# Kernel tuning notes

Hardware: AMD Instinct MI355X
Metric: run time of the kernel (lower is better)

Reference implementation:

```python
import jax, jax.numpy as jnp
import numpy as np

DX = 0.1
DY = 0.1
W_B = 1000.0
W_PARALLEL = 1000.0
W_DIV = 100.0
EPS = 1e-10


def setup_inputs() -> dict:
    key = jax.random.key(0)
    k1, k2 = jax.random.split(key)
    outputs = jax.random.normal(k1, (2, 3, 256, 256, 64), dtype=jnp.float32)
    targets = jax.random.normal(k2, (2, 4, 256, 256, 64), dtype=jnp.float32)
    return {"outputs": outputs, "targets": targets}


def _corners(f):
    # 8 shifted views f[..., i:, j:, k:] (with 0 -> [0:-1], 1 -> [1:]) on dims 2,3,4
    s0, s1 = slice(0, -1), slice(1, None)
    return {(i, j, k): f[:, :, (s1 if i else s0), (s1 if j else s0), (s1 if k else s0)]
            for i in (0, 1) for j in (0, 1) for k in (0, 1)}


def _forward(outputs, targets):
    bx_p, by_p, bz_p = outputs[:, 0:1], outputs[:, 1:2], outputs[:, 2:3]
    bx_t, by_t, bz_t = targets[:, 0:1], targets[:, 1:2], targets[:, 2:3]

    loss_b = (jnp.mean((bx_p**2 + by_p**2 - bx_t**2 - by_t**2) ** 2 / (bx_t**2 + by_t**2 + EPS))
              + jnp.mean((bz_p - bz_t) ** 4 / (bz_t**2 + EPS)))
    loss_parallel = jnp.mean((bx_p * by_t - by_p * bx_t) ** 2
                             / (bx_t**2 + by_t**2 + bz_t**2 + EPS))

    bx = _corners(bx_p)
    by = _corners(by_p)
    bz = _corners(bz_p)
    z = _corners(targets[:, 3:4])

    num = (0.25 * (bx[1, 0, 0] + bx[1, 1, 0] + bx[1, 0, 1] + bx[1, 1, 1]) * DY * 0.5 * (z[1, 0, 1] - z[1, 0, 0] + z[1, 1, 1] - z[1, 1, 0])
           - 0.25 * (bx[0, 0, 0] + bx[0, 1, 0] + bx[0, 0, 1] + bx[0, 1, 1]) * DY * 0.5 * (z[0, 0, 1] - z[0, 0, 0] + z[0, 1, 1] - z[0, 1, 0])
           + 0.25 * (by[0, 1, 0] + by[1, 1, 0] + by[0, 1, 1] + by[1, 1, 1]) * DX * 0.5 * (z[0, 1, 1] - z[0, 1, 0] + z[1, 1, 1] - z[1, 1, 0])
           - 0.25 * (by[0, 0, 0] + by[1, 0, 0] + by[0, 0, 1] + by[1, 0, 1]) * DX * 0.5 * (z[0, 0, 1] - z[0, 0, 0] + z[1, 0, 1] - z[1, 0, 0])
           + 0.25 * (bz[0, 0, 1] + bz[0, 1, 1] + bz[1, 0, 1] + bz[1, 1, 1]) * DX * DY
           - 0.25 * (bz[0, 0, 0] + bz[0, 1, 0] + bz[1, 0, 0] + bz[1, 1, 0]) * DX * DY
           + (bx[0, 0, 1] + bx[1, 0, 1] + bx[1, 1, 1]) * DY * (z[0, 0, 1] - z[1, 0, 1]) / 6
           + (bx[0, 1, 1] + bx[1, 1, 1] + bx[1, 0, 1]) * DY * (z[0, 1, 1] - z[1, 1, 1]) / 6
           + (by[1, 0, 1] + by[1, 1, 1] + by[0, 1, 1]) * DX * (z[1, 0, 1] - z[1, 1, 1]) / 6
           + (by[0, 0, 1] + by[0, 1, 1] + by[1, 1, 1]) * DX * (z[0, 0, 1] - z[0, 1, 1]) / 6
           - (bx[0, 0, 0] + bx[1, 0, 0] + bx[1, 1, 0]) * DY * (z[0, 0, 0] - z[1, 0, 0]) / 6
           - (bx[0, 1, 0] + bx[1, 1, 0] + bx[1, 0, 0]) * DY * (z[0, 1, 0] - z[1, 1, 0]) / 6
           - (by[1, 0, 0] + by[1, 1, 0] + by[0, 1, 0]) * DX * (z[1, 0, 0] - z[1, 1, 0]) / 6
           - (by[0, 0, 0] + by[0, 1, 0] + by[1, 1, 0]) * DX * (z[0, 0, 0] - z[0, 1, 0]) / 6)

    bx_c = sum(bx[c] for c in sorted(bx)) * 0.125
    by_c = sum(by[c] for c in sorted(by)) * 0.125
    bz_c = sum(bz[c] for c in sorted(bz)) * 0.125
    den = bx_c**2 + by_c**2 + bz_c**2 + EPS

    loss_div = jnp.mean(num**2 / den) / DX**2 / DY**2

    return (W_B * loss_b + W_PARALLEL * loss_parallel, W_DIV * loss_div)


def reference(outputs, targets):
    return _forward(outputs, targets)
```

## Files before the change

### kernel.cpp

```cpp
#include <hip/hip_runtime.h>

constexpr int B = 2, X = 256, Y = 256, Z = 64;
constexpr int CO = X * Y * Z;
constexpr int YZ = Y * Z;
constexpr long long N_PTS   = (long long)B * X * Y * Z;
constexpr long long M_CELLS = (long long)B * (X-1) * (Y-1) * (Z-1);

constexpr int ROWS = 4;
constexpr int SEGS = Y / ROWS;
constexpr int TPB  = 256;
constexpr int WPB  = TPB / 64;
constexpr int NSEG   = B * SEGS * X;
constexpr int BLOCKS = NSEG / WPB;

#define DXc 0.1f
#define DYc 0.1f
#define EPSc 1e-10f

#define F4C(v, c) (((c) == 0) ? (v).x : ((c) == 1) ? (v).y : ((c) == 2) ? (v).z : (v).w)

__global__ __launch_bounds__(TPB) void loss_main(const float* __restrict__ outs,
                                                 const float* __restrict__ tgts,
                                                 double* __restrict__ partial) {
    const int lane = threadIdx.x & 63;
    const int wv   = threadIdx.x >> 6;
    const int seg  = blockIdx.x * WPB + wv;

    const int b  = seg >> 14;
    const int r  = seg & 16383;
    const int sy = r >> 8;
    const int x  = r & 255;
    const int y0 = sy * ROWS;

    const int row = lane >> 4;
    const int zi  = (lane & 15) << 2;
    const int y_own = y0 + row;
    const int y_up  = (y_own + 1 < Y) ? (y_own + 1) : (Y - 1);

    const float* ob = outs + (size_t)b * 3 * CO;
    const float* tb = tgts + (size_t)b * 4 * CO;
    const int off00 = x * YZ + y_own * Z + zi;
    const int off01 = x * YZ + y_up  * Z + zi;
    const int off10 = off00 + YZ;
    const int off11 = off01 + YZ;

    #define LD4(p, off) (*(const float4*)((p) + (off)))

    double s_pt = 0.0;
    double s_dv = 0.0;

    const float4 obx = LD4(ob, 0 * CO + off00);
    const float4 oby = LD4(ob, 1 * CO + off00);
    const float4 obz = LD4(ob, 2 * CO + off00);
    const float4 tbx = LD4(tb, 0 * CO + off00);
    const float4 tby = LD4(tb, 1 * CO + off00);
    const float4 tbz = LD4(tb, 2 * CO + off00);
    const float4 tzc = LD4(tb, 3 * CO + off00);

    #pragma unroll
    for (int c = 0; c < 4; ++c) {
        const float bxp = F4C(obx, c), byp = F4C(oby, c), bzp = F4C(obz, c);
        const float bxt = F4C(tbx, c), byt = F4C(tby, c), bzt = F4C(tbz, c);
        const float bxt2 = bxt * bxt, byt2 = byt * byt, bzt2 = bzt * bzt;
        const float t1 = bxp * bxp + byp * byp - bxt2 - byt2;
        const float e1 = t1 * t1 / (bxt2 + byt2 + EPSc);
        const float dd = bzp - bzt;
        const float dd2 = dd * dd;
        const float e2 = dd2 * dd2 / (bzt2 + EPSc);
        const float cr = bxp * byt - byp * bxt;
        const float e3 = cr * cr / (bxt2 + byt2 + bzt2 + EPSc);
        s_pt += (double)(e1 + e2 + e3);
    }

    if (x < X - 1) {
        const float4 obx1  = LD4(ob, 0 * CO + off10);
        const float4 oby1  = LD4(ob, 1 * CO + off10);
        const float4 obz1  = LD4(ob, 2 * CO + off10);
        const float4 tzc1  = LD4(tb, 3 * CO + off10);
        const float4 obxy  = LD4(ob, 0 * CO + off01);
        const float4 obyy  = LD4(ob, 1 * CO + off01);
        const float4 obzy  = LD4(ob, 2 * CO + off01);
        const float4 tzcy  = LD4(tb, 3 * CO + off01);
        const float4 obxy1 = LD4(ob, 0 * CO + off11);
        const float4 obyy1 = LD4(ob, 1 * CO + off11);
        const float4 obzy1 = LD4(ob, 2 * CO + off11);
        const float4 tzcy1 = LD4(tb, 3 * CO + off11);

        const float n_obx   = __shfl_down(obx.x,   1);
        const float n_oby   = __shfl_down(oby.x,   1);
        const float n_obz   = __shfl_down(obz.x,   1);
        const float n_tzc   = __shfl_down(tzc.x,   1);
        const float n_obx1  = __shfl_down(obx1.x,  1);
        const float n_oby1  = __shfl_down(oby1.x,  1);
        const float n_obz1  = __shfl_down(obz1.x,  1);
        const float n_tzc1  = __shfl_down(tzc1.x,  1);
        const float n_obxy  = __shfl_down(obxy.x,  1);
        const float n_obyy  = __shfl_down(obyy.x,  1);
        const float n_obzy  = __shfl_down(obzy.x,  1);
        const float n_tzcy  = __shfl_down(tzcy.x,  1);
        const float n_obxy1 = __shfl_down(obxy1.x, 1);
        const float n_obyy1 = __shfl_down(obyy1.x, 1);
        const float n_obzy1 = __shfl_down(obzy1.x, 1);
        const float n_tzcy1 = __shfl_down(tzcy1.x, 1);

        const bool yvalid = (y_own < Y - 1);
        const float SIXTH = 1.0f / 6.0f;

        #pragma unroll
        for (int c = 0; c < 4; ++c) {
            const float bx000 = F4C(obx, c),   bx100 = F4C(obx1, c);
            const float bx010 = F4C(obxy, c),  bx110 = F4C(obxy1, c);
            const float by000 = F4C(oby, c),   by100 = F4C(oby1, c);
            const float by010 = F4C(obyy, c),  by110 = F4C(obyy1, c);
            const float bz000 = F4C(obz, c),   bz100 = F4C(obz1, c);
            const float bz010 = F4C(obzy, c),  bz110 = F4C(obzy1, c);
            const float zc000 = F4C(tzc, c),   zc100 = F4C(tzc1, c);
            const float zc010 = F4C(tzcy, c),  zc110 = F4C(tzcy1, c);

            const float bx001 = (c < 3) ? F4C(obx, c + 1)   : n_obx;
            const float bx101 = (c < 3) ? F4C(obx1, c + 1)  : n_obx1;
            const float bx011 = (c < 3) ? F4C(obxy, c + 1)  : n_obxy;
            const float bx111 = (c < 3) ? F4C(obxy1, c + 1) : n_obxy1;
            const float by001 = (c < 3) ? F4C(oby, c + 1)   : n_oby;
            const float by101 = (c < 3) ? F4C(oby1, c + 1)  : n_oby1;
            const float by011 = (c < 3) ? F4C(obyy, c + 1)  : n_obyy;
            const float by111 = (c < 3) ? F4C(obyy1, c + 1) : n_obyy1;
            const float bz001 = (c < 3) ? F4C(obz, c + 1)   : n_obz;
            const float bz101 = (c < 3) ? F4C(obz1, c + 1)  : n_obz1;
            const float bz011 = (c < 3) ? F4C(obzy, c + 1)  : n_obzy;
            const float bz111 = (c < 3) ? F4C(obzy1, c + 1) : n_obzy1;
            const float zc001 = (c < 3) ? F4C(tzc, c + 1)   : n_tzc;
            const float zc101 = (c < 3) ? F4C(tzc1, c + 1)  : n_tzc1;
            const float zc011 = (c < 3) ? F4C(tzcy, c + 1)  : n_tzcy;
            const float zc111 = (c < 3) ? F4C(tzcy1, c + 1) : n_tzcy1;

            const float num =
                  0.25f * (bx100 + bx110 + bx101 + bx111) * DYc * 0.5f * (zc101 - zc100 + zc111 - zc110)
                - 0.25f * (bx000 + bx010 + bx001 + bx011) * DYc * 0.5f * (zc001 - zc000 + zc011 - zc010)
                + 0.25f * (by010 + by110 + by011 + by111) * DXc * 0.5f * (zc011 - zc010 + zc111 - zc110)
                - 0.25f * (by000 + by100 + by001 + by101) * DXc * 0.5f * (zc001 - zc000 + zc101 - zc100)
                + 0.25f * (bz001 + bz011 + bz101 + bz111) * DXc * DYc
                - 0.25f * (bz000 + bz010 + bz100 + bz110) * DXc * DYc
                + (bx001 + bx101 + bx111) * DYc * (zc001 - zc101) * SIXTH
                + (bx011 + bx111 + bx101) * DYc * (zc011 - zc111) * SIXTH
                + (by101 + by111 + by011) * DXc * (zc101 - zc111) * SIXTH
                + (by001 + by011 + by111) * DXc * (zc001 - zc011) * SIXTH
                - (bx000 + bx100 + bx110) * DYc * (zc000 - zc100) * SIXTH
                - (bx010 + bx110 + bx100) * DYc * (zc010 - zc110) * SIXTH
                - (by100 + by110 + by010) * DXc * (zc100 - zc110) * SIXTH
                - (by000 + by010 + by110) * DXc * (zc000 - zc010) * SIXTH;

            const float bxc = 0.125f * (bx000 + bx100 + bx010 + bx110 + bx001 + bx101 + bx011 + bx111);
            const float byc = 0.125f * (by000 + by100 + by010 + by110 + by001 + by101 + by011 + by111);
            const float bzc = 0.125f * (bz000 + bz100 + bz010 + bz110 + bz001 + bz101 + bz011 + bz111);
            const float den = bxc * bxc + byc * byc + bzc * bzc + EPSc;

            const bool zvalid = (zi + c) < (Z - 1);
            if (yvalid && zvalid) {
                s_dv += (double)(num * num / den);
            }
        }
    }

    for (int off = 32; off > 0; off >>= 1) {
        s_pt += __shfl_down(s_pt, off);
        s_dv += __shfl_down(s_dv, off);
    }

    __shared__ double lds_pt[WPB];
    __shared__ double lds_dv[WPB];
    if (lane == 0) { lds_pt[wv] = s_pt; lds_dv[wv] = s_dv; }
    __syncthreads();
    if (threadIdx.x == 0) {
        double p = 0.0, d = 0.0;
        #pragma unroll
        for (int w = 0; w < WPB; ++w) { p += lds_pt[w]; d += lds_dv[w]; }
        partial[2 * blockIdx.x]     = p;
        partial[2 * blockIdx.x + 1] = d;
    }
}

__global__ __launch_bounds__(256) void loss_finalize(const double* __restrict__ partial,
                                                     float* __restrict__ out) {
    double s0 = 0.0, s1 = 0.0;
    for (int i = threadIdx.x; i < BLOCKS; i += 256) {
        s0 += partial[2 * i];
        s1 += partial[2 * i + 1];
    }
    const int lane = threadIdx.x & 63;
    const int wave = threadIdx.x >> 6;
    for (int off = 32; off > 0; off >>= 1) {
        s0 += __shfl_down(s0, off);
        s1 += __shfl_down(s1, off);
    }
    __shared__ double l0[4], l1[4];
    if (lane == 0) { l0[wave] = s0; l1[wave] = s1; }
    __syncthreads();
    if (threadIdx.x == 0) {
        double p = 0.0, d = 0.0;
        #pragma unroll
        for (int w = 0; w < 4; ++w) { p += l0[w]; d += l1[w]; }
        const double out0 = 1000.0 * (p / (double)N_PTS);
        const double out1 = 100.0 * (d / (double)M_CELLS) / (0.1 * 0.1) / (0.1 * 0.1);
        out[0] = (float)out0;
        out[1] = (float)out1;
    }
}

extern "C" void kernel_launch(void* const* d_in, const int* in_sizes, int n_in,
                              void* d_out, int out_size, void* d_ws, size_t ws_size,
                              hipStream_t stream) {
    const float* outs = (const float*)d_in[0];
    const float* tgts = (const float*)d_in[1];
    float* out = (float*)d_out;
    double* partial = (double*)d_ws;

    loss_main<<<BLOCKS, TPB, 0, stream>>>(outs, tgts, partial);
    loss_finalize<<<1, 256, 0, stream>>>(partial, out);
}
```

Baseline: 265.4 us.

## Refactor divergence stencil into per-z-plane partial sums with shuffled halo

Rewrites the divergence numerator into per-plane partial sums (x/y face sums, z differences, a per-plane G2 term) computed once per z index. The next plane comes from a single lane shuffle of the precomputed sums, replacing 16 raw-value shuffles and redundant adds. It also swaps divisions for hardware reciprocal approximations, accumulates per-thread sums in float before one double add, clamps x so all loads are issued up front, and sets launch_bounds occupancy. Risks are reduced precision from rcp and float accumulation, plus extra loads for edge rows.

Result: no change. 264.2 us (-0.5%).

```diff
diff --git a/kernel.cpp b/kernel.cpp
--- a/kernel.cpp
+++ b/kernel.cpp
@@ -13,15 +13,15 @@
 constexpr int NSEG   = B * SEGS * X;
 constexpr int BLOCKS = NSEG / WPB;
 
-#define DXc 0.1f
-#define DYc 0.1f
 #define EPSc 1e-10f
+#define SIXTH (1.0f / 6.0f)
+#define RCPF(v) __builtin_amdgcn_rcpf(v)
 
 #define F4C(v, c) (((c) == 0) ? (v).x : ((c) == 1) ? (v).y : ((c) == 2) ? (v).z : (v).w)
 
-__global__ __launch_bounds__(TPB) void loss_main(const float* __restrict__ outs,
-                                                 const float* __restrict__ tgts,
-                                                 double* __restrict__ partial) {
+__global__ __launch_bounds__(TPB, 4) void loss_main(const float* __restrict__ outs,
+                                                    const float* __restrict__ tgts,
+                                                    double* __restrict__ partial) {
     const int lane = threadIdx.x & 63;
     const int wv   = threadIdx.x >> 6;
     const int seg  = blockIdx.x * WPB + wv;
@@ -36,130 +36,122 @@
     const int zi  = (lane & 15) << 2;
     const int y_own = y0 + row;
     const int y_up  = (y_own + 1 < Y) ? (y_own + 1) : (Y - 1);
+    const int x_up  = (x + 1 < X) ? (x + 1) : (X - 1);
+    const bool xvalid = (x < X - 1);
+    const bool yvalid = (y_own < Y - 1);
 
     const float* ob = outs + (size_t)b * 3 * CO;
     const float* tb = tgts + (size_t)b * 4 * CO;
-    const int off00 = x * YZ + y_own * Z + zi;
-    const int off01 = x * YZ + y_up  * Z + zi;
-    const int off10 = off00 + YZ;
-    const int off11 = off01 + YZ;
+    const int off00 = x    * YZ + y_own * Z + zi;
+    const int off01 = x    * YZ + y_up  * Z + zi;
+    const int off10 = x_up * YZ + y_own * Z + zi;
+    const int off11 = x_up * YZ + y_up  * Z + zi;
 
     #define LD4(p, off) (*(const float4*)((p) + (off)))
+
+    const float4 obx   = LD4(ob, 0 * CO + off00);
+    const float4 oby   = LD4(ob, 1 * CO + off00);
+    const float4 obz   = LD4(ob, 2 * CO + off00);
+    const float4 tbx   = LD4(tb, 0 * CO + off00);
+    const float4 tby   = LD4(tb, 1 * CO + off00);
+    const float4 tbz   = LD4(tb, 2 * CO + off00);
+    const float4 tzc   = LD4(tb, 3 * CO + off00);
+    const float4 obx1  = LD4(ob, 0 * CO + off10);
+    const float4 oby1  = LD4(ob, 1 * CO + off10);
+    const float4 obz1  = LD4(ob, 2 * CO + off10);
+    const float4 tzc1  = LD4(tb, 3 * CO + off10);
+    const float4 obxy  = LD4(ob, 0 * CO + off01);
+    const float4 obyy  = LD4(ob, 1 * CO + off01);
+    const float4 obzy  = LD4(ob, 2 * CO + off01);
+    const float4 tzcy  = LD4(tb, 3 * CO + off01);
+    const float4 obxy1 = LD4(ob, 0 * CO + off11);
+    const float4 obyy1 = LD4(ob, 1 * CO + off11);
+    const float4 obzy1 = LD4(ob, 2 * CO + off11);
+    const float4 tzcy1 = LD4(tb, 3 * CO + off11);
 
     double s_pt = 0.0;
     double s_dv = 0.0;
 
-    const float4 obx = LD4(ob, 0 * CO + off00);
-    const float4 oby = LD4(ob, 1 * CO + off00);
-    const float4 obz = LD4(ob, 2 * CO + off00);
-    const float4 tbx = LD4(tb, 0 * CO + off00);
-    const float4 tby = LD4(tb, 1 * CO + off00);
-    const float4 tbz = LD4(tb, 2 * CO + off00);
-    const float4 tzc = LD4(tb, 3 * CO + off00);
-
-    #pragma unroll
-    for (int c = 0; c < 4; ++c) {
-        const float bxp = F4C(obx, c), byp = F4C(oby, c), bzp = F4C(obz, c);
-        const float bxt = F4C(tbx, c), byt = F4C(tby, c), bzt = F4C(tbz, c);
-        const float bxt2 = bxt * bxt, byt2 = byt * byt, bzt2 = bzt * bzt;
-        const float t1 = bxp * bxp + byp * byp - bxt2 - byt2;
-        const float e1 = t1 * t1 / (bxt2 + byt2 + EPSc);
-        const float dd = bzp - bzt;
-        const float dd2 = dd * dd;
-        const float e2 = dd2 * dd2 / (bzt2 + EPSc);
-        const float cr = bxp * byt - byp * bxt;
-        const float e3 = cr * cr / (bxt2 + byt2 + bzt2 + EPSc);
-        s_pt += (double)(e1 + e2 + e3);
-    }
-
-    if (x < X - 1) {
-        const float4 obx1  = LD4(ob, 0 * CO + off10);
-        const float4 oby1  = LD4(ob, 1 * CO + off10);
-        const float4 obz1  = LD4(ob, 2 * CO + off10);
-        const float4 tzc1  = LD4(tb, 3 * CO + off10);
-        const float4 obxy  = LD4(ob, 0 * CO + off01);
-        const float4 obyy  = LD4(ob, 1 * CO + off01);
-        const float4 obzy  = LD4(ob, 2 * CO + off01);
-        const float4 tzcy  = LD4(tb, 3 * CO + off01);
-        const float4 obxy1 = LD4(ob, 0 * CO + off11);
-        const float4 obyy1 = LD4(ob, 1 * CO + off11);
-        const float4 obzy1 = LD4(ob, 2 * CO + off11);
-        const float4 tzcy1 = LD4(tb, 3 * CO + off11);
-
-        const float n_obx   = __shfl_down(obx.x,   1);
-        const float n_oby   = __shfl_down(oby.x,   1);
-        const float n_obz   = __shfl_down(obz.x,   1);
-        const float n_tzc   = __shfl_down(tzc.x,   1);
-        const float n_obx1  = __shfl_down(obx1.x,  1);
-        const float n_oby1  = __shfl_down(oby1.x,  1);
-        const float n_obz1  = __shfl_down(obz1.x,  1);
-        const float n_tzc1  = __shfl_down(tzc1.x,  1);
-        const float n_obxy  = __shfl_down(obxy.x,  1);
-        const float n_obyy  = __shfl_down(obyy.x,  1);
-        const float n_obzy  = __shfl_down(obzy.x,  1);
-        const float n_tzcy  = __shfl_down(tzcy.x,  1);
-        const float n_obxy1 = __shfl_down(obxy1.x, 1);
-        const float n_obyy1 = __shfl_down(obyy1.x, 1);
-        const float n_obzy1 = __shfl_down(obzy1.x, 1);
-        const float n_tzcy1 = __shfl_down(tzcy1.x, 1);
-
-        const bool yvalid = (y_own < Y - 1);
-        const float SIXTH = 1.0f / 6.0f;
-
+    {
+        float pt4 = 0.0f;
         #pragma unroll
         for (int c = 0; c < 4; ++c) {
-            const float bx000 = F4C(obx, c),   bx100 = F4C(obx1, c);
-            const float bx010 = F4C(obxy, c),  bx110 = F4C(obxy1, c);
-            const float by000 = F4C(oby, c),   by100 = F4C(oby1, c);
-            const float by010 = F4C(obyy, c),  by110 = F4C(obyy1, c);
-            const float bz000 = F4C(obz, c),   bz100 = F4C(obz1, c);
-            const float bz010 = F4C(obzy, c),  bz110 = F4C(obzy1, c);
-            const float zc000 = F4C(tzc, c),   zc100 = F4C(tzc1, c);
-            const float zc010 = F4C(tzcy, c),  zc110 = F4C(tzcy1, c);
-
-            const float bx001 = (c < 3) ? F4C(obx, c + 1)   : n_obx;
-            const float bx101 = (c < 3) ? F4C(obx1, c + 1)  : n_obx1;
-            const float bx011 = (c < 3) ? F4C(obxy, c + 1)  : n_obxy;
-            const float bx111 = (c < 3) ? F4C(obxy1, c + 1) : n_obxy1;
-            const float by001 = (c < 3) ? F4C(oby, c + 1)   : n_oby;
-            const float by101 = (c < 3) ? F4C(oby1, c + 1)  : n_oby1;
-            const float by011 = (c < 3) ? F4C(obyy, c + 1)  : n_obyy;
-            const float by111 = (c < 3) ? F4C(obyy1, c + 1) : n_obyy1;
-            const float bz001 = (c < 3) ? F4C(obz, c + 1)   : n_obz;
-            const float bz101 = (c < 3) ? F4C(obz1, c + 1)  : n_obz1;
-            const float bz011 = (c < 3) ? F4C(obzy, c + 1)  : n_obzy;
-            const float bz111 = (c < 3) ? F4C(obzy1, c + 1) : n_obzy1;
-            const float zc001 = (c < 3) ? F4C(tzc, c + 1)   : n_tzc;
-            const float zc101 = (c < 3) ? F4C(tzc1, c + 1)  : n_tzc1;
-            const float zc011 = (c < 3) ? F4C(tzcy, c + 1)  : n_tzcy;
-            const float zc111 = (c < 3) ? F4C(tzcy1, c + 1) : n_tzcy1;
-
-            const float num =
-                  0.25f * (bx100 + bx110 + bx101 + bx111) * DYc * 0.5f * (zc101 - zc100 + zc111 - zc110)
-                - 0.25f * (bx000 + bx010 + bx001 + bx011) * DYc * 0.5f * (zc001 - zc000 + zc011 - zc010)
-                + 0.25f * (by010 + by110 + by011 + by111) * DXc * 0.5f * (zc011 - zc010 + zc111 - zc110)
-                - 0.25f * (by000 + by100 + by001 + by101) * DXc * 0.5f * (zc001 - zc000 + zc101 - zc100)
-                + 0.25f * (bz001 + bz011 + bz101 + bz111) * DXc * DYc
-                - 0.25f * (bz000 + bz010 + bz100 + bz110) * DXc * DYc
-                + (bx001 + bx101 + bx111) * DYc * (zc001 - zc101) * SIXTH
-                + (bx011 + bx111 + bx101) * DYc * (zc011 - zc111) * SIXTH
-                + (by101 + by111 + by011) * DXc * (zc101 - zc111) * SIXTH
-                + (by001 + by011 + by111) * DXc * (zc001 - zc011) * SIXTH
-                - (bx000 + bx100 + bx110) * DYc * (zc000 - zc100) * SIXTH
-                - (bx010 + bx110 + bx100) * DYc * (zc010 - zc110) * SIXTH
-                - (by100 + by110 + by010) * DXc * (zc100 - zc110) * SIXTH
-                - (by000 + by010 + by110) * DXc * (zc000 - zc010) * SIXTH;
-
-            const float bxc = 0.125f * (bx000 + bx100 + bx010 + bx110 + bx001 + bx101 + bx011 + bx111);
-            const float byc = 0.125f * (by000 + by100 + by010 + by110 + by001 + by101 + by011 + by111);
-            const float bzc = 0.125f * (bz000 + bz100 + bz010 + bz110 + bz001 + bz101 + bz011 + bz111);
-            const float den = bxc * bxc + byc * byc + bzc * bzc + EPSc;
-
-            const bool zvalid = (zi + c) < (Z - 1);
-            if (yvalid && zvalid) {
-                s_dv += (double)(num * num / den);
-            }
+            const float bxp = F4C(obx, c), byp = F4C(oby, c), bzp = F4C(obz, c);
+            const float bxt = F4C(tbx, c), byt = F4C(tby, c), bzt = F4C(tbz, c);
+            const float bxt2 = bxt * bxt, byt2 = byt * byt, bzt2 = bzt * bzt;
+            const float dxy = bxt2 + byt2;
+            const float t1 = bxp * bxp + byp * byp - dxy;
+            const float e1 = t1 * t1 * RCPF(dxy + EPSc);
+            const float dd = bzp - bzt;
+            const float dd2 = dd * dd;
+            const float e2 = dd2 * dd2 * RCPF(bzt2 + EPSc);
+            const float cr = bxp * byt - byp * bxt;
+            const float e3 = cr * cr * RCPF(dxy + bzt2 + EPSc);
+            pt4 += e1 + e2 + e3;
         }
+        s_pt += (double)pt4;
+    }
+
+    if (xvalid) {
+        float sxp[5], sxm[5], syp[5], sym[5];
+        float zxp[5], zxm[5], zyp[5], zym[5];
+        float Sx[5], Sy[5], Sz[5], G2[5];
+
+        #pragma unroll
+        for (int t = 0; t < 4; ++t) {
+            const float bx00 = F4C(obx, t),   bx10 = F4C(obx1, t);
+            const float bx01 = F4C(obxy, t),  bx11 = F4C(obxy1, t);
+            const float by00 = F4C(oby, t),   by10 = F4C(oby1, t);
+            const float by01 = F4C(obyy, t),  by11 = F4C(obyy1, t);
+            const float bz00 = F4C(obz, t),   bz10 = F4C(obz1, t);
+            const float bz01 = F4C(obzy, t),  bz11 = F4C(obzy1, t);
+            const float zc00 = F4C(tzc, t),   zc10 = F4C(tzc1, t);
+            const float zc01 = F4C(tzcy, t),  zc11 = F4C(tzcy1, t);
+
+            sxp[t] = bx10 + bx11;   sxm[t] = bx00 + bx01;
+            syp[t] = by01 + by11;   sym[t] = by00 + by10;
+            zxp[t] = zc10 + zc11;   zxm[t] = zc00 + zc01;
+            zyp[t] = zc01 + zc11;   zym[t] = zc00 + zc10;
+            Sx[t] = sxp[t] + sxm[t];
+            Sy[t] = syp[t] + sym[t];
+            Sz[t] = (bz00 + bz01) + (bz10 + bz11);
+            G2[t] = 0.025f * Sz[t]
+                  + SIXTH * ((bx00 + sxp[t]) * (zc00 - zc10)
+                           + (bx01 + sxp[t]) * (zc01 - zc11)
+                           + (by10 + syp[t]) * (zc10 - zc11)
+                           + (by00 + syp[t]) * (zc00 - zc01));
+        }
+        sxp[4] = __shfl_down(sxp[0], 1);
+        sxm[4] = __shfl_down(sxm[0], 1);
+        syp[4] = __shfl_down(syp[0], 1);
+        sym[4] = __shfl_down(sym[0], 1);
+        zxp[4] = __shfl_down(zxp[0], 1);
+        zxm[4] = __shfl_down(zxm[0], 1);
+        zyp[4] = __shfl_down(zyp[0], 1);
+        zym[4] = __shfl_down(zym[0], 1);
+        Sz[4]  = __shfl_down(Sz[0],  1);
+        G2[4]  = __shfl_down(G2[0],  1);
+        Sx[4] = sxp[4] + sxm[4];
+        Sy[4] = syp[4] + sym[4];
+
+        float dv4 = 0.0f;
+        #pragma unroll
+        for (int c = 0; c < 4; ++c) {
+            const float fx = (sxp[c] + sxp[c+1]) * (zxp[c+1] - zxp[c])
+                           - (sxm[c] + sxm[c+1]) * (zxm[c+1] - zxm[c])
+                           + (syp[c] + syp[c+1]) * (zyp[c+1] - zyp[c])
+                           - (sym[c] + sym[c+1]) * (zym[c+1] - zym[c]);
+            const float num2 = 0.125f * fx + (G2[c+1] - G2[c]);
+            const float SxS = Sx[c] + Sx[c+1];
+            const float SyS = Sy[c] + Sy[c+1];
+            const float SzS = Sz[c] + Sz[c+1];
+            const float q = SxS * SxS + SyS * SyS + SzS * SzS;
+            const float den = 0.015625f * q + EPSc;
+            const float v = num2 * num2 * RCPF(den);
+            const bool ok = yvalid && ((zi + c) < Z - 1);
+            dv4 += ok ? v : 0.0f;
+        }
+        s_dv += (double)dv4;
     }
 
     for (int off = 32; off > 0; off >>= 1) {
@@ -201,7 +193,7 @@
         #pragma unroll
         for (int w = 0; w < 4; ++w) { p += l0[w]; d += l1[w]; }
         const double out0 = 1000.0 * (p / (double)N_PTS);
-        const double out1 = 100.0 * (d / (double)M_CELLS) / (0.1 * 0.1) / (0.1 * 0.1);
+        const double out1 = 10000.0 * (d / (double)M_CELLS);
         out[0] = (float)out0;
         out[1] = (float)out1;
     }
```
